# Optimization experiments

Measured on AMD Instinct MI355X. Metric: run time of the kernel, lower is better.

The kernel has to match this reference:

```python
import jax, jax.numpy as jnp
import numpy as np

B, L, D, N, H = 2, 2048, 1024, 16, 64  # batch, seq, d_model, heads, head_dim


def setup_inputs() -> dict:
    key = jax.random.key(0)
    k_x, k_qkv, k_proj = jax.random.split(key, 3)
    x = jax.random.normal(k_x, (B, L, D), dtype=jnp.float32)
    # RoPE table (L, H//2, 2) holding (cos, sin) per position/frequency
    inv_freq = 1.0 / (10000.0 ** (jnp.arange(H // 2, dtype=jnp.float32) / (H // 2)))
    ang = jnp.arange(L, dtype=jnp.float32)[:, None] * inv_freq[None, :]  # (L, H//2)
    rope = jnp.stack([jnp.cos(ang), jnp.sin(ang)], axis=-1)  # (L, H//2, 2)
    mask = jnp.tril(jnp.ones((L, L), dtype=bool))[None, None]  # (1,1,L,L) causal
    w_qkv = jax.random.normal(k_qkv, (D, 3 * D), dtype=jnp.float32) * 0.02
    w_proj = jax.random.normal(k_proj, (D, D), dtype=jnp.float32) * 0.02
    return {"x": x, "rope": rope, "mask": mask, "w_qkv": w_qkv, "w_proj": w_proj}


def _apply_rope(t, rope):
    # t: (B, L, N, H), rope: (L, H//2, 2)
    b, l, n, h = t.shape
    tp = t.reshape(b, l, n, h // 2, 2)
    cos = rope[None, :, None, :, 0]  # (1, L, 1, H//2)
    sin = rope[None, :, None, :, 1]
    t0, t1 = tp[..., 0], tp[..., 1]
    out = jnp.stack([t0 * cos - t1 * sin, t0 * sin + t1 * cos], axis=-1)
    return out.reshape(b, l, n, h)


def reference(x, rope, mask, w_qkv, w_proj):
    b, l, d = x.shape
    h = rope.shape[1] * 2
    n = d // h
    qkv = x @ w_qkv  # (b, l, 3d)
    q, k, v = jnp.split(qkv, 3, axis=2)
    q = _apply_rope(q.reshape(b, l, n, h), rope)
    k = _apply_rope(k.reshape(b, l, n, h), rope)
    v = v.reshape(b, l, n, h)
    scale = 1.0 / jnp.sqrt(jnp.asarray(h, dtype=x.dtype))
    scores = jnp.einsum('blnh,bmnh->bnlm', q, k) * scale  # (b, n, l, l)
    scores = jnp.where(mask, scores, jnp.finfo(scores.dtype).min)
    attn = jax.nn.softmax(scores, axis=-1)
    out = jnp.einsum('bnlm,bmnh->blnh', attn, v).reshape(b, l, d)
    return out @ w_proj
```

## Files before the change

kernel.cpp:

```cpp
#include <hip/hip_runtime.h>
#include <cmath>
#include <cstdint>


typedef __attribute__((ext_vector_type(8))) short bfrag8;
typedef __attribute__((ext_vector_type(4))) float f32x4;
typedef __attribute__((ext_vector_type(8))) unsigned short u16x8;

#define AS1 __attribute__((address_space(1)))
#define AS3 __attribute__((address_space(3)))

__device__ __forceinline__ unsigned short f2bf(float f) {
  uint32_t u = __builtin_bit_cast(uint32_t, f);
  u += 0x7fffu + ((u >> 16) & 1u);
  return (unsigned short)(u >> 16);
}
__device__ __forceinline__ float bf2f(unsigned short h) {
  return __builtin_bit_cast(float, (uint32_t)h << 16);
}
__device__ __forceinline__ int swz(int row, int bytecol) {
  return row * 128 + (bytecol ^ ((row & 7) << 4));
}

__global__ __launch_bounds__(256)
void f32_to_bf16_vec(const float* __restrict__ in, unsigned short* __restrict__ out, int n) {
  const int i = (blockIdx.x * 256 + threadIdx.x) * 4;
  if (i < n) {
    float4 v = *reinterpret_cast<const float4*>(in + i);
    ushort4 o;
    o.x = f2bf(v.x); o.y = f2bf(v.y); o.z = f2bf(v.z); o.w = f2bf(v.w);
    *reinterpret_cast<ushort4*>(out + i) = o;
  }
}

__global__ __launch_bounds__(256)
void transpose_f32_to_bf16(const float* __restrict__ w, unsigned short* __restrict__ wT,
                           int R, int C) {
  __shared__ float t[32][33];
  const int tx = threadIdx.x & 31, ty = threadIdx.x >> 5;
  const int c0 = blockIdx.x * 32, r0 = blockIdx.y * 32;
  #pragma unroll
  for (int s = 0; s < 32; s += 8)
    t[ty + s][tx] = w[(size_t)(r0 + ty + s) * C + c0 + tx];
  __syncthreads();
  #pragma unroll
  for (int s = 0; s < 32; s += 8)
    wT[(size_t)(c0 + ty + s) * R + r0 + tx] = f2bf(t[tx][ty + s]);
}

__global__ __launch_bounds__(256)
void gemm_bt_bf16(const unsigned short* __restrict__ A, const unsigned short* __restrict__ Bt,
                  void* __restrict__ C0, unsigned short* __restrict__ C1,
                  int K, int ldC0, int ldC1, int splitcol, int bf16_out) {
  __shared__ __align__(16) unsigned short As[128 * 64];
  __shared__ __align__(16) unsigned short Bs[128 * 64];

  const int tid  = threadIdx.x;
  const int brow = blockIdx.y * 128;
  const int bcol = blockIdx.x * 128;
  const int wid  = tid >> 6, lane = tid & 63;
  const int wr = (wid >> 1) * 64;
  const int wc = (wid & 1) * 64;
  const int lrow = lane & 15;
  const int lko  = (lane >> 4) * 8;
  const int srow  = tid >> 3;
  const int skoff = (tid & 7) * 8;

  f32x4 acc[4][4];
  #pragma unroll
  for (int m = 0; m < 4; ++m)
    #pragma unroll
    for (int n = 0; n < 4; ++n) acc[m][n] = (f32x4){0.f, 0.f, 0.f, 0.f};

  for (int k0 = 0; k0 < K; k0 += 64) {
    __syncthreads();
    #pragma unroll
    for (int i = 0; i < 4; ++i) {
      const int r = i * 32 + srow;
      __builtin_amdgcn_global_load_lds(
          (const AS1 void*)(A + (size_t)(brow + r) * K + k0 + skoff),
          (AS3 void*)(As + r * 64 + skoff), 16, 0, 0);
      __builtin_amdgcn_global_load_lds(
          (const AS1 void*)(Bt + (size_t)(bcol + r) * K + k0 + skoff),
          (AS3 void*)(Bs + r * 64 + skoff), 16, 0, 0);
    }
    __syncthreads();

    #pragma unroll
    for (int ks = 0; ks < 2; ++ks) {
      bfrag8 a[4], b[4];
      #pragma unroll
      for (int m = 0; m < 4; ++m)
        a[m] = *reinterpret_cast<const bfrag8*>(&As[(wr + m * 16 + lrow) * 64 + ks * 32 + lko]);
      #pragma unroll
      for (int n = 0; n < 4; ++n)
        b[n] = *reinterpret_cast<const bfrag8*>(&Bs[(wc + n * 16 + lrow) * 64 + ks * 32 + lko]);
      #pragma unroll
      for (int m = 0; m < 4; ++m)
        #pragma unroll
        for (int n = 0; n < 4; ++n)
          acc[m][n] = __builtin_amdgcn_mfma_f32_16x16x32_bf16(a[m], b[n], acc[m][n], 0, 0, 0);
    }
  }

  const int crow0 = brow + wr + (lane >> 4) * 4;
  const int ccol0 = bcol + wc + lrow;
  if (bcol >= splitcol) {
    unsigned short* C = C1;
    const int cc = ccol0 - splitcol;
    #pragma unroll
    for (int m = 0; m < 4; ++m)
      #pragma unroll
      for (int n = 0; n < 4; ++n)
        #pragma unroll
        for (int r = 0; r < 4; ++r)
          C[(size_t)(crow0 + m * 16 + r) * ldC1 + cc + n * 16] = f2bf(acc[m][n][r]);
  } else if (bf16_out) {
    unsigned short* C = (unsigned short*)C0;
    #pragma unroll
    for (int m = 0; m < 4; ++m)
      #pragma unroll
      for (int n = 0; n < 4; ++n)
        #pragma unroll
        for (int r = 0; r < 4; ++r)
          C[(size_t)(crow0 + m * 16 + r) * ldC0 + ccol0 + n * 16] = f2bf(acc[m][n][r]);
  } else {
    float* C = (float*)C0;
    #pragma unroll
    for (int m = 0; m < 4; ++m)
      #pragma unroll
      for (int n = 0; n < 4; ++n)
        #pragma unroll
        for (int r = 0; r < 4; ++r)
          C[(size_t)(crow0 + m * 16 + r) * ldC0 + ccol0 + n * 16] = acc[m][n][r];
  }
}

__global__ __launch_bounds__(256)
void rope_qk_kernel(const unsigned short* __restrict__ qk,
                    const float* __restrict__ rope,
                    unsigned short* __restrict__ Qr, unsigned short* __restrict__ Kr) {
  const int t = blockIdx.x * 256 + threadIdx.x;
  const int row = t >> 7;
  const int c8 = (t & 127) << 3;
  const int l = row & 2047;
  const float2* rp = (const float2*)rope + (size_t)l * 32 + ((c8 & 63) >> 1);

  u16x8 q = *reinterpret_cast<const u16x8*>(qk + (size_t)row * 2048 + c8);
  u16x8 k = *reinterpret_cast<const u16x8*>(qk + (size_t)row * 2048 + 1024 + c8);
  u16x8 qo, ko;
  #pragma unroll
  for (int p = 0; p < 4; ++p) {
    const float2 cs = rp[p];
    float q0 = bf2f(q[2 * p]), q1 = bf2f(q[2 * p + 1]);
    qo[2 * p]     = f2bf((q0 * cs.x - q1 * cs.y) * 0.125f);
    qo[2 * p + 1] = f2bf((q0 * cs.y + q1 * cs.x) * 0.125f);
    float k0 = bf2f(k[2 * p]), k1 = bf2f(k[2 * p + 1]);
    ko[2 * p]     = f2bf(k0 * cs.x - k1 * cs.y);
    ko[2 * p + 1] = f2bf(k0 * cs.y + k1 * cs.x);
  }
  *reinterpret_cast<u16x8*>(Qr + (size_t)row * 1024 + c8) = qo;
  *reinterpret_cast<u16x8*>(Kr + (size_t)row * 1024 + c8) = ko;
}

__global__ __launch_bounds__(256)
void v_transpose_kernel(const unsigned short* __restrict__ Vbuf,
                        unsigned short* __restrict__ Vt) {
  __shared__ unsigned short t[64][72];
  const int lt = blockIdx.x;
  const int bn = blockIdx.y;
  const int b = bn >> 4, n = bn & 15;
  const int r = threadIdx.x >> 2;
  const int cb = (threadIdx.x & 3) << 4;

  const unsigned short* src = Vbuf + (size_t)b * 2048 * 1024 + n * 64;
  #pragma unroll
  for (int c = 0; c < 2; ++c) {
    u16x8 v = *reinterpret_cast<const u16x8*>(src + (size_t)(lt * 64 + r) * 1024 + cb + c * 8);
    *reinterpret_cast<u16x8*>(&t[r][cb + c * 8]) = v;
  }
  __syncthreads();
  unsigned short* dst = Vt + ((size_t)bn * 64 + r) * 2048 + lt * 64;
  #pragma unroll
  for (int c = 0; c < 2; ++c) {
    u16x8 o;
    #pragma unroll
    for (int j = 0; j < 8; ++j) o[j] = t[cb + c * 8 + j][r];
    *reinterpret_cast<u16x8*>(dst + cb + c * 8) = o;
  }
}

__global__ __launch_bounds__(256)
void attn_mfma_kernel(const unsigned short* __restrict__ Qr,
                      const unsigned short* __restrict__ Kr,
                      const unsigned short* __restrict__ Vt,
                      unsigned short* __restrict__ out) {
  __shared__ __align__(16) unsigned short PQ_s[64 * 64];
  __shared__ __align__(16) unsigned short K_s[2][64 * 64];
  __shared__ __align__(16) unsigned short V_s[2][64 * 64];

  const int tid = threadIdx.x;
  const int wid = tid >> 6, lane = tid & 63;
  const int lrow = lane & 15;
  const int lko  = (lane >> 4) * 8;
  const int i_blk = blockIdx.x;
  const int qt = (i_blk < 512) ? (31 - (i_blk >> 5)) : ((i_blk - 512) >> 5);
  const int bn = i_blk & 31;
  const int b = bn >> 4, n = bn & 15;

  const unsigned short* qb = Qr + (size_t)b * 2048 * 1024 + n * 64;
  const unsigned short* kb = Kr + (size_t)b * 2048 * 1024 + n * 64;
  const unsigned short* vb = Vt + (size_t)bn * 64 * 2048;
  unsigned short* ob = out + (size_t)b * 2048 * 1024 + n * 64;

  const int srow = lane >> 3;
  const int sgr  = (lane & 7) ^ srow;

  #pragma unroll
  for (int i = 0; i < 2; ++i) {
    const int row = i * 32 + wid * 8 + srow;
    __builtin_amdgcn_global_load_lds(
        (const AS1 void*)(qb + (size_t)(qt * 64 + row) * 1024 + sgr * 8),
        (AS3 void*)(PQ_s + (i * 32 + wid * 8) * 64 + lane * 8), 16, 0, 0);
    __builtin_amdgcn_global_load_lds(
        (const AS1 void*)(kb + (size_t)(0 * 64 + row) * 1024 + sgr * 8),
        (AS3 void*)(&K_s[0][(i * 32 + wid * 8) * 64 + lane * 8]), 16, 0, 0);
    __builtin_amdgcn_global_load_lds(
        (const AS1 void*)(vb + (size_t)row * 2048 + 0 * 64 + sgr * 8),
        (AS3 void*)(&V_s[0][(i * 32 + wid * 8) * 64 + lane * 8]), 16, 0, 0);
  }
  __syncthreads();

  bfrag8 aq[2];
  #pragma unroll
  for (int ks = 0; ks < 2; ++ks)
    aq[ks] = *reinterpret_cast<const bfrag8*>(
        (const char*)PQ_s + swz(wid * 16 + lrow, (ks * 32 + lko) * 2));

  f32x4 oa[4];
  float l_r[4];
  #pragma unroll
  for (int r = 0; r < 4; ++r) l_r[r] = 0.f;
  #pragma unroll
  for (int nn = 0; nn < 4; ++nn) oa[nn] = (f32x4){0.f, 0.f, 0.f, 0.f};

  int cur = 0;
  for (int kt = 0; kt <= qt; ++kt) {
    if (kt < qt) {
      #pragma unroll
      for (int i = 0; i < 2; ++i) {
        const int row = i * 32 + wid * 8 + srow;
        __builtin_amdgcn_global_load_lds(
            (const AS1 void*)(kb + (size_t)((kt + 1) * 64 + row) * 1024 + sgr * 8),
            (AS3 void*)(&K_s[cur ^ 1][(i * 32 + wid * 8) * 64 + lane * 8]), 16, 0, 0);
        __builtin_amdgcn_global_load_lds(
            (const AS1 void*)(vb + (size_t)row * 2048 + (kt + 1) * 64 + sgr * 8),
            (AS3 void*)(&V_s[cur ^ 1][(i * 32 + wid * 8) * 64 + lane * 8]), 16, 0, 0);
      }
    }
    const char* Kb = (const char*)&K_s[cur][0];
    const char* Vb = (const char*)&V_s[cur][0];

    f32x4 s[4];
    #pragma unroll
    for (int nn = 0; nn < 4; ++nn) s[nn] = (f32x4){0.f, 0.f, 0.f, 0.f};
    __builtin_amdgcn_s_setprio(1);
    #pragma unroll
    for (int ks = 0; ks < 2; ++ks) {
      #pragma unroll
      for (int nn = 0; nn < 4; ++nn) {
        bfrag8 bk = *reinterpret_cast<const bfrag8*>(Kb + swz(nn * 16 + lrow, (ks * 32 + lko) * 2));
        s[nn] = __builtin_amdgcn_mfma_f32_16x16x32_bf16(aq[ks], bk, s[nn], 0, 0, 0);
      }
    }
    __builtin_amdgcn_s_setprio(0);

    const bool diag = (kt == qt);
    #pragma unroll
    for (int r = 0; r < 4; ++r) {
      const int lrow_q = wid * 16 + (lane >> 4) * 4 + r;
      #pragma unroll
      for (int nn = 0; nn < 4; ++nn) {
        float v = s[nn][r];
        if (diag && (nn * 16 + lrow) > lrow_q) v = -INFINITY;
        const float p = __expf(v);
        const unsigned short pbf = f2bf(p);
        l_r[r] += bf2f(pbf);
        *(unsigned short*)((char*)PQ_s + swz(lrow_q, (nn * 16 + lrow) * 2)) = pbf;
      }
    }

    __builtin_amdgcn_s_setprio(1);
    #pragma unroll
    for (int ks = 0; ks < 2; ++ks) {
      bfrag8 pa = *reinterpret_cast<const bfrag8*>(
          (const char*)PQ_s + swz(wid * 16 + lrow, (ks * 32 + lko) * 2));
      #pragma unroll
      for (int nn = 0; nn < 4; ++nn) {
        bfrag8 bv = *reinterpret_cast<const bfrag8*>(Vb + swz(nn * 16 + lrow, (ks * 32 + lko) * 2));
        oa[nn] = __builtin_amdgcn_mfma_f32_16x16x32_bf16(pa, bv, oa[nn], 0, 0, 0);
      }
    }
    __builtin_amdgcn_s_setprio(0);

    __syncthreads();
    cur ^= 1;
  }

  unsigned short* op = ob + (size_t)(qt * 64 + wid * 16 + (lane >> 4) * 4) * 1024;
  #pragma unroll
  for (int r = 0; r < 4; ++r) {
    float rs = l_r[r];
    rs += __shfl_xor(rs, 1);
    rs += __shfl_xor(rs, 2);
    rs += __shfl_xor(rs, 4);
    rs += __shfl_xor(rs, 8);
    const float inv = 1.f / rs;
    #pragma unroll
    for (int nn = 0; nn < 4; ++nn)
      op[(size_t)r * 1024 + nn * 16 + lrow] = f2bf(oa[nn][r] * inv);
  }
}

extern "C" void kernel_launch(void* const* d_in, const int* in_sizes, int n_in,
                              void* d_out, int out_size, void* d_ws, size_t ws_size,
                              hipStream_t stream) {
  (void)in_sizes; (void)n_in; (void)out_size; (void)ws_size;
  const float* x      = (const float*)d_in[0];
  const float* rope   = (const float*)d_in[1];
  const float* w_qkv  = (const float*)d_in[3];
  const float* w_proj = (const float*)d_in[4];
  float* out = (float*)d_out;

  const size_t MB = 1u << 20;
  char* ws = (char*)d_ws;
  unsigned short* x_bf   = (unsigned short*)(ws);
  unsigned short* Qrp    = (unsigned short*)(ws);
  unsigned short* wqkvT  = (unsigned short*)(ws + 8 * MB);
  unsigned short* Krp    = (unsigned short*)(ws + 8 * MB);
  unsigned short* qk     = (unsigned short*)(ws + 16 * MB);
  unsigned short* Vtp    = (unsigned short*)(ws + 16 * MB);
  unsigned short* Vbuf   = (unsigned short*)(ws + 32 * MB);
  unsigned short* wprojT = (unsigned short*)(ws + 32 * MB);
  unsigned short* attn   = (unsigned short*)(ws + 34 * MB);

  f32_to_bf16_vec<<<4096, 256, 0, stream>>>(x, x_bf, 4096 * 1024);
  transpose_f32_to_bf16<<<dim3(96, 32), 256, 0, stream>>>(w_qkv, wqkvT, 1024, 3072);

  gemm_bt_bf16<<<dim3(24, 32), 256, 0, stream>>>(x_bf, wqkvT, qk, Vbuf,
                                                 1024, 2048, 1024, 2048, 1);

  rope_qk_kernel<<<2048, 256, 0, stream>>>(qk, rope, Qrp, Krp);
  v_transpose_kernel<<<dim3(32, 32), 256, 0, stream>>>(Vbuf, Vtp);

  transpose_f32_to_bf16<<<dim3(32, 32), 256, 0, stream>>>(w_proj, wprojT, 1024, 1024);

  attn_mfma_kernel<<<1024, 256, 0, stream>>>(Qrp, Krp, Vtp, attn);

  gemm_bt_bf16<<<dim3(8, 32), 256, 0, stream>>>(attn, wprojT, out, nullptr,
                                                1024, 1024, 0, 1 << 30, 0);
}
```

Measured before the change: 223.7 us.

## Fuse RoPE into QKV GEMM epilogue and remap GEMM blocks for L2 locality

Removes the separate RoPE kernel by applying the rotary embedding, and the query scale, in the QKV GEMM epilogue. Pair partners are exchanged with lane shuffles and Q/K are written directly as bf16. This drops one kernel launch and a round trip of the intermediate QK buffer through memory. The GEMM also switches to a 1D grid with a swizzled block-to-tile mapping meant to improve cache reuse. The workspace is reorganized, and the w_proj transpose is moved earlier in the launch sequence.

```diff
diff --git a/kernel.cpp b/kernel.cpp
--- a/kernel.cpp
+++ b/kernel.cpp
@@ -48,16 +48,21 @@
     wT[(size_t)(c0 + ty + s) * R + r0 + tx] = f2bf(t[tx][ty + s]);
 }
 
+template <int MODE>
 __global__ __launch_bounds__(256)
 void gemm_bt_bf16(const unsigned short* __restrict__ A, const unsigned short* __restrict__ Bt,
                   void* __restrict__ C0, unsigned short* __restrict__ C1,
-                  int K, int ldC0, int ldC1, int splitcol, int bf16_out) {
+                  unsigned short* __restrict__ Qr, unsigned short* __restrict__ Kr,
+                  const float* __restrict__ rope, int K) {
   __shared__ __align__(16) unsigned short As[128 * 64];
   __shared__ __align__(16) unsigned short Bs[128 * 64];
 
+  const int wg = blockIdx.x;
+  const int szid = (wg & 7) * (gridDim.x >> 3) + (wg >> 3);
+  const int brow = (szid & 31) * 128;
+  const int bcol = (szid >> 5) * 128;
+
   const int tid  = threadIdx.x;
-  const int brow = blockIdx.y * 128;
-  const int bcol = blockIdx.x * 128;
   const int wid  = tid >> 6, lane = tid & 63;
   const int wr = (wid >> 1) * 64;
   const int wc = (wid & 1) * 64;
@@ -105,62 +110,52 @@
 
   const int crow0 = brow + wr + (lane >> 4) * 4;
   const int ccol0 = bcol + wc + lrow;
-  if (bcol >= splitcol) {
-    unsigned short* C = C1;
-    const int cc = ccol0 - splitcol;
+
+  if (MODE == 0) {
+    float* C = (float*)C0;
     #pragma unroll
     for (int m = 0; m < 4; ++m)
       #pragma unroll
       for (int n = 0; n < 4; ++n)
         #pragma unroll
         for (int r = 0; r < 4; ++r)
-          C[(size_t)(crow0 + m * 16 + r) * ldC1 + cc + n * 16] = f2bf(acc[m][n][r]);
-  } else if (bf16_out) {
-    unsigned short* C = (unsigned short*)C0;
-    #pragma unroll
-    for (int m = 0; m < 4; ++m)
-      #pragma unroll
-      for (int n = 0; n < 4; ++n)
+          C[(size_t)(crow0 + m * 16 + r) * 1024 + ccol0 + n * 16] = acc[m][n][r];
+  } else {
+    if (bcol >= 2048) {
+      const int cc = ccol0 - 2048;
+      #pragma unroll
+      for (int m = 0; m < 4; ++m)
         #pragma unroll
-        for (int r = 0; r < 4; ++r)
-          C[(size_t)(crow0 + m * 16 + r) * ldC0 + ccol0 + n * 16] = f2bf(acc[m][n][r]);
-  } else {
-    float* C = (float*)C0;
-    #pragma unroll
-    for (int m = 0; m < 4; ++m)
-      #pragma unroll
-      for (int n = 0; n < 4; ++n)
+        for (int n = 0; n < 4; ++n)
+          #pragma unroll
+          for (int r = 0; r < 4; ++r)
+            C1[(size_t)(crow0 + m * 16 + r) * 1024 + cc + n * 16] = f2bf(acc[m][n][r]);
+    } else {
+      const bool isq = (bcol < 1024);
+      unsigned short* T = isq ? Qr : Kr;
+      const int cb = bcol + wc + lrow - (isq ? 0 : 1024);
+      const float sc = isq ? 0.125f : 1.0f;
+      const int odd = lane & 1;
+      const int pio = lrow >> 1;
+      #pragma unroll
+      for (int m = 0; m < 4; ++m) {
         #pragma unroll
-        for (int r = 0; r < 4; ++r)
-          C[(size_t)(crow0 + m * 16 + r) * ldC0 + ccol0 + n * 16] = acc[m][n][r];
-  }
-}
-
-__global__ __launch_bounds__(256)
-void rope_qk_kernel(const unsigned short* __restrict__ qk,
-                    const float* __restrict__ rope,
-                    unsigned short* __restrict__ Qr, unsigned short* __restrict__ Kr) {
-  const int t = blockIdx.x * 256 + threadIdx.x;
-  const int row = t >> 7;
-  const int c8 = (t & 127) << 3;
-  const int l = row & 2047;
-  const float2* rp = (const float2*)rope + (size_t)l * 32 + ((c8 & 63) >> 1);
-
-  u16x8 q = *reinterpret_cast<const u16x8*>(qk + (size_t)row * 2048 + c8);
-  u16x8 k = *reinterpret_cast<const u16x8*>(qk + (size_t)row * 2048 + 1024 + c8);
-  u16x8 qo, ko;
-  #pragma unroll
-  for (int p = 0; p < 4; ++p) {
-    const float2 cs = rp[p];
-    float q0 = bf2f(q[2 * p]), q1 = bf2f(q[2 * p + 1]);
-    qo[2 * p]     = f2bf((q0 * cs.x - q1 * cs.y) * 0.125f);
-    qo[2 * p + 1] = f2bf((q0 * cs.y + q1 * cs.x) * 0.125f);
-    float k0 = bf2f(k[2 * p]), k1 = bf2f(k[2 * p + 1]);
-    ko[2 * p]     = f2bf(k0 * cs.x - k1 * cs.y);
-    ko[2 * p + 1] = f2bf(k0 * cs.y + k1 * cs.x);
-  }
-  *reinterpret_cast<u16x8*>(Qr + (size_t)row * 1024 + c8) = qo;
-  *reinterpret_cast<u16x8*>(Kr + (size_t)row * 1024 + c8) = ko;
+        for (int r = 0; r < 4; ++r) {
+          const int grow = crow0 + m * 16 + r;
+          const float2* rrow = (const float2*)rope + (size_t)(grow & 2047) * 32;
+          #pragma unroll
+          for (int n = 0; n < 4; ++n) {
+            const float v  = acc[m][n][r];
+            const float pv = __shfl_xor(v, 1);
+            const float2 cs = rrow[n * 8 + pio];
+            const float o = odd ? fmaf(pv, cs.y, v * cs.x)
+                                : fmaf(v, cs.x, -(pv * cs.y));
+            T[(size_t)grow * 1024 + cb + n * 16] = f2bf(o * sc);
+          }
+        }
+      }
+    }
+  }
 }
 
 __global__ __launch_bounds__(256)
@@ -335,28 +330,25 @@
   const size_t MB = 1u << 20;
   char* ws = (char*)d_ws;
   unsigned short* x_bf   = (unsigned short*)(ws);
-  unsigned short* Qrp    = (unsigned short*)(ws);
+  unsigned short* attn   = (unsigned short*)(ws);
   unsigned short* wqkvT  = (unsigned short*)(ws + 8 * MB);
-  unsigned short* Krp    = (unsigned short*)(ws + 8 * MB);
-  unsigned short* qk     = (unsigned short*)(ws + 16 * MB);
-  unsigned short* Vtp    = (unsigned short*)(ws + 16 * MB);
-  unsigned short* Vbuf   = (unsigned short*)(ws + 32 * MB);
-  unsigned short* wprojT = (unsigned short*)(ws + 32 * MB);
-  unsigned short* attn   = (unsigned short*)(ws + 34 * MB);
+  unsigned short* Qrp    = (unsigned short*)(ws + 14 * MB);
+  unsigned short* Krp    = (unsigned short*)(ws + 22 * MB);
+  unsigned short* Vbuf   = (unsigned short*)(ws + 30 * MB);
+  unsigned short* Vtp    = (unsigned short*)(ws + 38 * MB);
+  unsigned short* wprojT = (unsigned short*)(ws + 46 * MB);
 
   f32_to_bf16_vec<<<4096, 256, 0, stream>>>(x, x_bf, 4096 * 1024);
   transpose_f32_to_bf16<<<dim3(96, 32), 256, 0, stream>>>(w_qkv, wqkvT, 1024, 3072);
-
-  gemm_bt_bf16<<<dim3(24, 32), 256, 0, stream>>>(x_bf, wqkvT, qk, Vbuf,
-                                                 1024, 2048, 1024, 2048, 1);
-
-  rope_qk_kernel<<<2048, 256, 0, stream>>>(qk, rope, Qrp, Krp);
+  transpose_f32_to_bf16<<<dim3(32, 32), 256, 0, stream>>>(w_proj, wprojT, 1024, 1024);
+
+  gemm_bt_bf16<1><<<768, 256, 0, stream>>>(x_bf, wqkvT, nullptr, Vbuf,
+                                           Qrp, Krp, rope, 1024);
+
   v_transpose_kernel<<<dim3(32, 32), 256, 0, stream>>>(Vbuf, Vtp);
 
-  transpose_f32_to_bf16<<<dim3(32, 32), 256, 0, stream>>>(w_proj, wprojT, 1024, 1024);
-
   attn_mfma_kernel<<<1024, 256, 0, stream>>>(Qrp, Krp, Vtp, attn);
 
-  gemm_bt_bf16<<<dim3(8, 32), 256, 0, stream>>>(attn, wprojT, out, nullptr,
-                                                1024, 1024, 0, 1 << 30, 0);
-}
+  gemm_bt_bf16<0><<<256, 256, 0, stream>>>(attn, wprojT, out, nullptr,
+                                           nullptr, nullptr, nullptr, 1024);
+}
```

After: 225.2 us. About the same (+0.7%).
